# Kernel tuning notes

Hardware: AMD Instinct MI355X
Metric: run time of the kernel (lower is better)

## Reference

```python
import jax, jax.numpy as jnp
import numpy as np

NUM_HEADS = 12
EMB = 768
HEAD = 64
SEQ = 2048
BATCH = 2


def setup_inputs() -> dict:
    key = jax.random.key(0)
    ks = jax.random.split(key, 6)
    scale = 0.02
    x = jax.random.normal(ks[0], (BATCH, SEQ, EMB), dtype=jnp.float32)
    # per-head Q/K/V projections (bias-free, Karpathy-style HeadAttention), batched over heads
    Wq = jax.random.normal(ks[1], (NUM_HEADS, EMB, HEAD), dtype=jnp.float32) * scale
    Wk = jax.random.normal(ks[2], (NUM_HEADS, EMB, HEAD), dtype=jnp.float32) * scale
    Wv = jax.random.normal(ks[3], (NUM_HEADS, EMB, HEAD), dtype=jnp.float32) * scale
    # output projection: Linear(head_size*num_heads, emb_size)
    Wo = jax.random.normal(ks[4], (NUM_HEADS * HEAD, EMB), dtype=jnp.float32) * scale
    bo = jax.random.normal(ks[5], (EMB,), dtype=jnp.float32) * scale
    return {"x": x, "Wq": Wq, "Wk": Wk, "Wv": Wv, "Wo": Wo, "bo": bo}


def reference(x, Wq, Wk, Wv, Wo, bo):
    B, S, E = x.shape
    # batched per-head projections: [B,S,E] x [H,E,D] -> [B,H,S,D]
    q = jnp.einsum("bse,hed->bhsd", x, Wq)
    k = jnp.einsum("bse,hed->bhsd", x, Wk)
    v = jnp.einsum("bse,hed->bhsd", x, Wv)
    scale = 1.0 / jnp.sqrt(jnp.asarray(HEAD, dtype=x.dtype))
    scores = jnp.einsum("bhsd,bhtd->bhst", q, k) * scale  # [B,H,S,S]
    causal = jnp.tril(jnp.ones((S, S), dtype=bool))
    scores = jnp.where(causal, scores, jnp.asarray(-jnp.inf, dtype=scores.dtype))
    attn = jax.nn.softmax(scores, axis=-1)
    out = jnp.einsum("bhst,bhtd->bhsd", attn, v)  # [B,H,S,D]
    # concat heads along last dim: [B,S,H*D]
    out = out.transpose(0, 2, 1, 3).reshape(B, S, NUM_HEADS * HEAD)
    # output projection (dropout is identity in eval mode)
    return out @ Wo + bo
```

## Files before the change

### kernel.cpp

```cpp
#include <hip/hip_runtime.h>

#define NHEAD 12
#define EMB 768
#define HDD 64
#define SEQ 2048

typedef __attribute__((ext_vector_type(4))) float f32x4;
typedef __attribute__((ext_vector_type(8))) short short8;
typedef unsigned int u32;

#define GLL16(g, l)                                                            \
    __builtin_amdgcn_global_load_lds(                                          \
        (const __attribute__((address_space(1))) u32*)(g),                     \
        (__attribute__((address_space(3))) u32*)(l), 16, 0, 0)

static __device__ __forceinline__ short bf16s(float f) {
    unsigned u = __builtin_bit_cast(unsigned, f);
    u = (u + 0x7fffu + ((u >> 16) & 1u)) >> 16;
    return (short)u;
}

__global__ void k_cvt_x(const float* __restrict__ x, short* __restrict__ xb) {
    const int i = (blockIdx.x * 256 + threadIdx.x) * 8;
    const f32x4* s = (const f32x4*)(x + i);
    f32x4 a = s[0], b = s[1];
    short8 o;
    o[0] = bf16s(a[0]); o[1] = bf16s(a[1]); o[2] = bf16s(a[2]); o[3] = bf16s(a[3]);
    o[4] = bf16s(b[0]); o[5] = bf16s(b[1]); o[6] = bf16s(b[2]); o[7] = bf16s(b[3]);
    *(short8*)(xb + i) = o;
}

__global__ void k_cvt_whead(const float* __restrict__ Wq, const float* __restrict__ Wk,
                            const float* __restrict__ Wv, short* __restrict__ WqT,
                            short* __restrict__ WkT, short* __restrict__ WvT) {
    const float* W = blockIdx.z == 0 ? Wq : (blockIdx.z == 1 ? Wk : Wv);
    short* Wt = blockIdx.z == 0 ? WqT : (blockIdx.z == 1 ? WkT : WvT);
    __shared__ float tile[64][65];
    const int h = blockIdx.x, e0 = blockIdx.y * 64;
    const int t = threadIdx.x;
    const int r = t >> 2, c0 = (t & 3) * 16;
    const float* src = W + (h * EMB + e0 + r) * HDD + c0;
#pragma unroll
    for (int i = 0; i < 16; ++i) tile[r][c0 + i] = src[i];
    __syncthreads();
    short* dst = Wt + (h * HDD + r) * EMB + e0 + c0;
#pragma unroll
    for (int i = 0; i < 16; ++i) dst[i] = bf16s(tile[c0 + i][r]);
}

__global__ void k_cvt_wo(const float* __restrict__ W, short* __restrict__ Wt) {
    __shared__ float tile[64][65];
    const int k0 = blockIdx.x * 64, n0 = blockIdx.y * 64;
    const int t = threadIdx.x;
    const int r = t >> 2, c0 = (t & 3) * 16;
    const float* src = W + (k0 + r) * EMB + n0 + c0;
#pragma unroll
    for (int i = 0; i < 16; ++i) tile[r][c0 + i] = src[i];
    __syncthreads();
    short* dst = Wt + (n0 + r) * EMB + k0 + c0;
#pragma unroll
    for (int i = 0; i < 16; ++i) dst[i] = bf16s(tile[c0 + i][r]);
}

template <int MODE>
__global__ __launch_bounds__(256) void k_gemm(
        const short* __restrict__ xb, const short* __restrict__ Wt0,
        const short* __restrict__ Wt1, const short* __restrict__ Wt2,
        short* __restrict__ Qo, short* __restrict__ Ko, short* __restrict__ Vo,
        const float* __restrict__ bias, float* __restrict__ Fout) {
    __shared__ alignas(16) short As[128 * 32];
    __shared__ alignas(16) short Bs[128 * 32];
    const int t = threadIdx.x, lane = t & 63, wave = t >> 6;
    const int z = (MODE == 0) ? blockIdx.z : 0;
    const short* Ap;
    const short* Bp;
    int m0, n0;
    if (MODE == 1) {
        Ap = xb; Bp = Wt0; m0 = blockIdx.y * 128; n0 = blockIdx.x * 128;
    } else if (z == 0) {
        Ap = xb; Bp = Wt0; m0 = blockIdx.y * 128; n0 = blockIdx.x * 128;
    } else if (z == 1) {
        Ap = xb; Bp = Wt1; m0 = blockIdx.y * 128; n0 = blockIdx.x * 128;
    } else {
        Ap = Wt2; Bp = xb; m0 = blockIdx.x * 128; n0 = blockIdx.y * 128;
    }

    const short* gA = Ap + (long)(m0 + wave * 32 + (lane >> 2)) * EMB + (lane & 3) * 8;
    const short* gB = Bp + (long)(n0 + wave * 32 + (lane >> 2)) * EMB + (lane & 3) * 8;
    short* lA = As + (wave * 32) * 32;
    short* lB = Bs + (wave * 32) * 32;

    const int wm = (wave >> 1) * 64, wn = (wave & 1) * 64;
    const int fr = lane & 15, hi = lane >> 4, fk = hi * 8;

    f32x4 acc[4][4];
#pragma unroll
    for (int i = 0; i < 4; ++i)
#pragma unroll
        for (int j = 0; j < 4; ++j)
#pragma unroll
            for (int e = 0; e < 4; ++e) acc[i][j][e] = 0.f;

    for (int kk = 0; kk < EMB; kk += 32) {
        __syncthreads();
        GLL16(gA + kk, lA);
        GLL16(gA + kk + 16 * EMB, lA + 16 * 32);
        GLL16(gB + kk, lB);
        GLL16(gB + kk + 16 * EMB, lB + 16 * 32);
        __syncthreads();
        short8 af[4], bfq[4];
#pragma unroll
        for (int i = 0; i < 4; ++i)
            af[i] = *(const short8*)(As + (wm + i * 16 + fr) * 32 + fk);
#pragma unroll
        for (int j = 0; j < 4; ++j)
            bfq[j] = *(const short8*)(Bs + (wn + j * 16 + fr) * 32 + fk);
#pragma unroll
        for (int i = 0; i < 4; ++i)
#pragma unroll
            for (int j = 0; j < 4; ++j)
                acc[i][j] = __builtin_amdgcn_mfma_f32_16x16x32_bf16(af[i], bfq[j], acc[i][j], 0, 0, 0);
    }

    const int r0 = hi * 4;
#pragma unroll
    for (int i = 0; i < 4; ++i) {
#pragma unroll
        for (int j = 0; j < 4; ++j) {
            const int nbase = n0 + wn + j * 16 + fr;
            float bj = 0.f;
            if (MODE == 1) bj = bias[nbase];
#pragma unroll
            for (int r = 0; r < 4; ++r) {
                const int m = m0 + wm + i * 16 + r0 + r;
                float v = acc[i][j][r];
                if (MODE == 0) {
                    if (z == 2) {
                        const int hh = m >> 6, dd = m & 63;
                        const int bb = nbase >> 11, ss = nbase & 2047;
                        Vo[(long)((bb * NHEAD + hh) * HDD + dd) * SEQ + ss] = bf16s(v);
                    } else {
                        const int bb = m >> 11, ss = m & 2047;
                        const int hh = nbase >> 6, dd = nbase & 63;
                        short* Dst = (z == 0) ? Qo : Ko;
                        if (z == 0) v *= 0.125f;
                        Dst[(long)((bb * NHEAD + hh) * SEQ + ss) * HDD + dd] = bf16s(v);
                    }
                } else {
                    Fout[(long)m * EMB + nbase] = v + bj;
                }
            }
        }
    }
}

__global__ __launch_bounds__(512) void k_attn(
        const short* __restrict__ Q, const short* __restrict__ K,
        const short* __restrict__ VT, short* __restrict__ O) {
    __shared__ alignas(16) short Kbuf[2][64 * 72];
    __shared__ alignas(16) short Vbuf[2][64 * 72];
    __shared__ alignas(16) short Ps[8][16 * 72];
    const int bh = blockIdx.x;
    const int h = bh % NHEAD, b = bh / NHEAD;
    const int qs = (int)gridDim.y - 1 - (int)blockIdx.y;
    const int q0 = qs * 128;
    const int ntile = 2 * qs + 2;
    const int t = threadIdx.x, lane = t & 63, wave = t >> 6;
    const long base = (long)(b * NHEAD + h) * SEQ * HDD;
    const short* Qg = Q + base;
    const short* Kg = K + base;
    const short* Vg = VT + base;
    const int fr = lane & 15, hi = lane >> 4, fk = hi * 8, r0 = hi * 4;
    const int wq = q0 + wave * 16;

    short8 qf[2];
#pragma unroll
    for (int c = 0; c < 2; ++c)
        qf[c] = *(const short8*)(Qg + (long)(wq + fr) * HDD + c * 32 + fk);

    f32x4 oacc[4];
#pragma unroll
    for (int i = 0; i < 4; ++i)
#pragma unroll
        for (int e = 0; e < 4; ++e) oacc[i][e] = 0.f;
    float mrun = -3e38f, lrun = 0.f;

    const int srow = t >> 3, scol = (t & 7) * 8;
    const short* KgS = Kg + (long)srow * HDD + scol;
    const short* VgS = Vg + (long)srow * SEQ + scol;
    short* Pw = &Ps[wave][0];

    short8 kvR = *(const short8*)(KgS);
    short8 vvR = *(const short8*)(VgS);
    *(short8*)(&Kbuf[0][srow * 72 + scol]) = kvR;
    *(short8*)(&Vbuf[0][srow * 72 + scol]) = vvR;
    if (ntile > 1) {
        kvR = *(const short8*)(KgS + (long)64 * HDD);
        vvR = *(const short8*)(VgS + 64);
    }
    __syncthreads();

    for (int kt = 0; kt < ntile; ++kt) {
        const int k0 = kt * 64;
        const int cur = kt & 1;
        if (kt + 1 < ntile) {
            *(short8*)(&Kbuf[cur ^ 1][srow * 72 + scol]) = kvR;
            *(short8*)(&Vbuf[cur ^ 1][srow * 72 + scol]) = vvR;
            if (kt + 2 < ntile) {
                kvR = *(const short8*)(KgS + (long)(k0 + 128) * HDD);
                vvR = *(const short8*)(VgS + (k0 + 128));
            }
        }
        if (k0 <= wq + 15) {
            const short* Ks = &Kbuf[cur][0];
            const short* Vs = &Vbuf[cur][0];

            f32x4 st[4];
#pragma unroll
            for (int nt = 0; nt < 4; ++nt) {
                const short8 kf0 = *(const short8*)(Ks + (nt * 16 + fr) * 72 + fk);
                const short8 kf1 = *(const short8*)(Ks + (nt * 16 + fr) * 72 + 32 + fk);
#pragma unroll
                for (int e = 0; e < 4; ++e) st[nt][e] = 0.f;
                st[nt] = __builtin_amdgcn_mfma_f32_16x16x32_bf16(kf0, qf[0], st[nt], 0, 0, 0);
                st[nt] = __builtin_amdgcn_mfma_f32_16x16x32_bf16(kf1, qf[1], st[nt], 0, 0, 0);
            }

            float p[4][4];
            float pmax = -3e38f;
            if (k0 + 63 > wq) {
                const int myq = wq + fr;
#pragma unroll
                for (int nt = 0; nt < 4; ++nt)
#pragma unroll
                    for (int r = 0; r < 4; ++r) {
                        float s = st[nt][r];
                        if (k0 + nt * 16 + r0 + r > myq) s = -3e38f;
                        p[nt][r] = s;
                        pmax = fmaxf(pmax, s);
                    }
            } else {
#pragma unroll
                for (int nt = 0; nt < 4; ++nt)
#pragma unroll
                    for (int r = 0; r < 4; ++r) {
                        p[nt][r] = st[nt][r];
                        pmax = fmaxf(pmax, st[nt][r]);
                    }
            }
            pmax = fmaxf(pmax, __shfl_xor(pmax, 16, 64));
            pmax = fmaxf(pmax, __shfl_xor(pmax, 32, 64));
            const float mnew = fmaxf(mrun, pmax);
            const float corr = __expf(mrun - mnew);
            mrun = mnew;
            float rsum = 0.f;
#pragma unroll
            for (int nt = 0; nt < 4; ++nt)
#pragma unroll
                for (int r = 0; r < 4; ++r) {
                    const float e = __expf(p[nt][r] - mnew);
                    p[nt][r] = e;
                    rsum += e;
                }
            rsum += __shfl_xor(rsum, 16, 64);
            rsum += __shfl_xor(rsum, 32, 64);
            lrun = lrun * corr + rsum;
#pragma unroll
            for (int dt = 0; dt < 4; ++dt)
#pragma unroll
                for (int e = 0; e < 4; ++e) oacc[dt][e] *= corr;

#pragma unroll
            for (int nt = 0; nt < 4; ++nt)
#pragma unroll
                for (int r = 0; r < 4; ++r)
                    Pw[fr * 72 + nt * 16 + r0 + r] = bf16s(p[nt][r]);

#pragma unroll
            for (int kc = 0; kc < 2; ++kc) {
                const short8 pf = *(const short8*)(Pw + fr * 72 + kc * 32 + fk);
#pragma unroll
                for (int dt = 0; dt < 4; ++dt) {
                    const short8 vf = *(const short8*)(Vs + (dt * 16 + fr) * 72 + kc * 32 + fk);
                    oacc[dt] = __builtin_amdgcn_mfma_f32_16x16x32_bf16(vf, pf, oacc[dt], 0, 0, 0);
                }
            }
        }
        __syncthreads();
    }

    short* Os = &Ps[0][0];
    const float iv = 1.0f / lrun;
#pragma unroll
    for (int dt = 0; dt < 4; ++dt)
#pragma unroll
        for (int r = 0; r < 4; ++r)
            Os[(wave * 16 + fr) * 72 + dt * 16 + r0 + r] = bf16s(oacc[dt][r] * iv);
    __syncthreads();
    {
        const int row = t >> 2, c0 = (t & 3) * 16;
        const short8 o0 = *(const short8*)(Os + row * 72 + c0);
        const short8 o1 = *(const short8*)(Os + row * 72 + c0 + 8);
        short* Og = O + (long)(b * SEQ + q0 + row) * EMB + h * HDD + c0;
        *(short8*)Og = o0;
        *(short8*)(Og + 8) = o1;
    }
}

extern "C" void kernel_launch(void* const* d_in, const int* in_sizes, int n_in,
                              void* d_out, int out_size, void* d_ws, size_t ws_size,
                              hipStream_t stream) {
    const float* x  = (const float*)d_in[0];
    const float* Wq = (const float*)d_in[1];
    const float* Wk = (const float*)d_in[2];
    const float* Wv = (const float*)d_in[3];
    const float* Wo = (const float*)d_in[4];
    const float* bo = (const float*)d_in[5];
    float* out = (float*)d_out;

    char* ws = (char*)d_ws;
    short* xb  = (short*)(ws + 0);
    short* WqT = (short*)(ws + 6291456);
    short* WkT = (short*)(ws + 7471104);
    short* WvT = (short*)(ws + 8650752);
    short* WoT = (short*)(ws + 9830400);
    short* Qb  = (short*)(ws + 11010048);
    short* Kb  = (short*)(ws + 17301504);
    short* VTb = (short*)(ws + 23592960);
    short* Ob  = (short*)(ws + 29884416);

    k_cvt_x<<<dim3(1536), dim3(256), 0, stream>>>(x, xb);
    k_cvt_whead<<<dim3(12, 12, 3), dim3(256), 0, stream>>>(Wq, Wk, Wv, WqT, WkT, WvT);
    k_cvt_wo<<<dim3(12, 12), dim3(256), 0, stream>>>(Wo, WoT);
    k_gemm<0><<<dim3(6, 32, 3), dim3(256), 0, stream>>>(
        xb, WqT, WkT, WvT, Qb, Kb, VTb, (const float*)nullptr, (float*)nullptr);
    k_attn<<<dim3(24, 16), dim3(512), 0, stream>>>(Qb, Kb, VTb, Ob);
    k_gemm<1><<<dim3(6, 32, 1), dim3(256), 0, stream>>>(
        Ob, WoT, (const short*)nullptr, (const short*)nullptr,
        (short*)nullptr, (short*)nullptr, (short*)nullptr, bo, out);
}
```

Measured before the change: 106.8 us.

## Widen GEMM K-tile with XOR-swizzled LDS, pair causal query blocks in attention

```diff
diff --git a/kernel.cpp b/kernel.cpp
--- a/kernel.cpp
+++ b/kernel.cpp
@@ -7,6 +7,7 @@
 
 typedef __attribute__((ext_vector_type(4))) float f32x4;
 typedef __attribute__((ext_vector_type(8))) short short8;
+typedef __attribute__((ext_vector_type(4))) short short4v;
 typedef unsigned int u32;
 
 #define GLL16(g, l)                                                            \
@@ -62,14 +63,15 @@
     for (int i = 0; i < 16; ++i) dst[i] = bf16s(tile[c0 + i][r]);
 }
 
+#define GBK 64
 template <int MODE>
 __global__ __launch_bounds__(256) void k_gemm(
         const short* __restrict__ xb, const short* __restrict__ Wt0,
         const short* __restrict__ Wt1, const short* __restrict__ Wt2,
         short* __restrict__ Qo, short* __restrict__ Ko, short* __restrict__ Vo,
         const float* __restrict__ bias, float* __restrict__ Fout) {
-    __shared__ alignas(16) short As[128 * 32];
-    __shared__ alignas(16) short Bs[128 * 32];
+    __shared__ alignas(16) short As[128 * GBK];
+    __shared__ alignas(16) short Bs[128 * GBK];
     const int t = threadIdx.x, lane = t & 63, wave = t >> 6;
     const int z = (MODE == 0) ? blockIdx.z : 0;
     const short* Ap;
@@ -85,13 +87,14 @@
         Ap = Wt2; Bp = xb; m0 = blockIdx.x * 128; n0 = blockIdx.y * 128;
     }
 
-    const short* gA = Ap + (long)(m0 + wave * 32 + (lane >> 2)) * EMB + (lane & 3) * 8;
-    const short* gB = Bp + (long)(n0 + wave * 32 + (lane >> 2)) * EMB + (lane & 3) * 8;
-    short* lA = As + (wave * 32) * 32;
-    short* lB = Bs + (wave * 32) * 32;
+    const int srow = lane >> 3;
+    const int scolSw = ((lane & 7) ^ (lane >> 3)) * 8;
+    const short* gA = Ap + (long)(m0 + wave * 32 + srow) * EMB + scolSw;
+    const short* gB = Bp + (long)(n0 + wave * 32 + srow) * EMB + scolSw;
 
     const int wm = (wave >> 1) * 64, wn = (wave & 1) * 64;
     const int fr = lane & 15, hi = lane >> 4, fk = hi * 8;
+    const int sxa = (fr & 7) << 3;
 
     f32x4 acc[4][4];
 #pragma unroll
@@ -101,25 +104,29 @@
 #pragma unroll
             for (int e = 0; e < 4; ++e) acc[i][j][e] = 0.f;
 
-    for (int kk = 0; kk < EMB; kk += 32) {
-        __syncthreads();
-        GLL16(gA + kk, lA);
-        GLL16(gA + kk + 16 * EMB, lA + 16 * 32);
-        GLL16(gB + kk, lB);
-        GLL16(gB + kk + 16 * EMB, lB + 16 * 32);
-        __syncthreads();
-        short8 af[4], bfq[4];
-#pragma unroll
-        for (int i = 0; i < 4; ++i)
-            af[i] = *(const short8*)(As + (wm + i * 16 + fr) * 32 + fk);
-#pragma unroll
-        for (int j = 0; j < 4; ++j)
-            bfq[j] = *(const short8*)(Bs + (wn + j * 16 + fr) * 32 + fk);
-#pragma unroll
-        for (int i = 0; i < 4; ++i)
+    for (int kk = 0; kk < EMB; kk += GBK) {
+        __syncthreads();
+#pragma unroll
+        for (int i = 0; i < 4; ++i) {
+            GLL16(gA + kk + i * 8 * EMB, As + (wave * 32 + i * 8) * GBK);
+            GLL16(gB + kk + i * 8 * EMB, Bs + (wave * 32 + i * 8) * GBK);
+        }
+        __syncthreads();
+#pragma unroll
+        for (int kc = 0; kc < GBK; kc += 32) {
+            short8 af[4], bfq[4];
+#pragma unroll
+            for (int i = 0; i < 4; ++i)
+                af[i] = *(const short8*)(As + (wm + i * 16 + fr) * GBK + ((kc + fk) ^ sxa));
 #pragma unroll
             for (int j = 0; j < 4; ++j)
-                acc[i][j] = __builtin_amdgcn_mfma_f32_16x16x32_bf16(af[i], bfq[j], acc[i][j], 0, 0, 0);
+                bfq[j] = *(const short8*)(Bs + (wn + j * 16 + fr) * GBK + ((kc + fk) ^ sxa));
+#pragma unroll
+            for (int i = 0; i < 4; ++i)
+#pragma unroll
+                for (int j = 0; j < 4; ++j)
+                    acc[i][j] = __builtin_amdgcn_mfma_f32_16x16x32_bf16(af[i], bfq[j], acc[i][j], 0, 0, 0);
+        }
     }
 
     const int r0 = hi * 4;
@@ -162,148 +169,157 @@
     __shared__ alignas(16) short Ps[8][16 * 72];
     const int bh = blockIdx.x;
     const int h = bh % NHEAD, b = bh / NHEAD;
-    const int qs = (int)gridDim.y - 1 - (int)blockIdx.y;
-    const int q0 = qs * 128;
-    const int ntile = 2 * qs + 2;
+    const int pairp = blockIdx.y;
     const int t = threadIdx.x, lane = t & 63, wave = t >> 6;
     const long base = (long)(b * NHEAD + h) * SEQ * HDD;
     const short* Qg = Q + base;
     const short* Kg = K + base;
     const short* Vg = VT + base;
     const int fr = lane & 15, hi = lane >> 4, fk = hi * 8, r0 = hi * 4;
-    const int wq = q0 + wave * 16;
-
-    short8 qf[2];
-#pragma unroll
-    for (int c = 0; c < 2; ++c)
-        qf[c] = *(const short8*)(Qg + (long)(wq + fr) * HDD + c * 32 + fk);
-
-    f32x4 oacc[4];
-#pragma unroll
-    for (int i = 0; i < 4; ++i)
-#pragma unroll
-        for (int e = 0; e < 4; ++e) oacc[i][e] = 0.f;
-    float mrun = -3e38f, lrun = 0.f;
-
     const int srow = t >> 3, scol = (t & 7) * 8;
     const short* KgS = Kg + (long)srow * HDD + scol;
     const short* VgS = Vg + (long)srow * SEQ + scol;
     short* Pw = &Ps[wave][0];
-
-    short8 kvR = *(const short8*)(KgS);
-    short8 vvR = *(const short8*)(VgS);
-    *(short8*)(&Kbuf[0][srow * 72 + scol]) = kvR;
-    *(short8*)(&Vbuf[0][srow * 72 + scol]) = vvR;
-    if (ntile > 1) {
-        kvR = *(const short8*)(KgS + (long)64 * HDD);
-        vvR = *(const short8*)(VgS + 64);
-    }
-    __syncthreads();
-
-    for (int kt = 0; kt < ntile; ++kt) {
-        const int k0 = kt * 64;
-        const int cur = kt & 1;
-        if (kt + 1 < ntile) {
-            *(short8*)(&Kbuf[cur ^ 1][srow * 72 + scol]) = kvR;
-            *(short8*)(&Vbuf[cur ^ 1][srow * 72 + scol]) = vvR;
-            if (kt + 2 < ntile) {
-                kvR = *(const short8*)(KgS + (long)(k0 + 128) * HDD);
-                vvR = *(const short8*)(VgS + (k0 + 128));
+    short* Os = &Ps[0][0];
+
+#pragma unroll
+    for (int ph = 0; ph < 2; ++ph) {
+        const int qs = ph == 0 ? 15 - pairp : pairp;
+        const int q0 = qs * 128;
+        const int ntile = 2 * qs + 2;
+        const int wq = q0 + wave * 16;
+
+        short8 qf[2];
+#pragma unroll
+        for (int c = 0; c < 2; ++c)
+            qf[c] = *(const short8*)(Qg + (long)(wq + fr) * HDD + c * 32 + fk);
+
+        f32x4 oacc[4];
+#pragma unroll
+        for (int i = 0; i < 4; ++i)
+#pragma unroll
+            for (int e = 0; e < 4; ++e) oacc[i][e] = 0.f;
+        float mrun = -3e38f, lrun = 0.f;
+
+        short8 kvR = *(const short8*)(KgS);
+        short8 vvR = *(const short8*)(VgS);
+        *(short8*)(&Kbuf[0][srow * 72 + scol]) = kvR;
+        *(short8*)(&Vbuf[0][srow * 72 + scol]) = vvR;
+        if (ntile > 1) {
+            kvR = *(const short8*)(KgS + (long)64 * HDD);
+            vvR = *(const short8*)(VgS + 64);
+        }
+        __syncthreads();
+
+        for (int kt = 0; kt < ntile; ++kt) {
+            const int k0 = kt * 64;
+            const int cur = kt & 1;
+            if (kt + 1 < ntile) {
+                *(short8*)(&Kbuf[cur ^ 1][srow * 72 + scol]) = kvR;
+                *(short8*)(&Vbuf[cur ^ 1][srow * 72 + scol]) = vvR;
+                if (kt + 2 < ntile) {
+                    kvR = *(const short8*)(KgS + (long)(k0 + 128) * HDD);
+                    vvR = *(const short8*)(VgS + (k0 + 128));
+                }
             }
-        }
-        if (k0 <= wq + 15) {
-            const short* Ks = &Kbuf[cur][0];
-            const short* Vs = &Vbuf[cur][0];
-
-            f32x4 st[4];
-#pragma unroll
-            for (int nt = 0; nt < 4; ++nt) {
-                const short8 kf0 = *(const short8*)(Ks + (nt * 16 + fr) * 72 + fk);
-                const short8 kf1 = *(const short8*)(Ks + (nt * 16 + fr) * 72 + 32 + fk);
-#pragma unroll
-                for (int e = 0; e < 4; ++e) st[nt][e] = 0.f;
-                st[nt] = __builtin_amdgcn_mfma_f32_16x16x32_bf16(kf0, qf[0], st[nt], 0, 0, 0);
-                st[nt] = __builtin_amdgcn_mfma_f32_16x16x32_bf16(kf1, qf[1], st[nt], 0, 0, 0);
+            if (k0 <= wq + 15) {
+                const short* Ks = &Kbuf[cur][0];
+                const short* Vs = &Vbuf[cur][0];
+
+                f32x4 st[4];
+#pragma unroll
+                for (int nt = 0; nt < 4; ++nt) {
+                    const short8 kf0 = *(const short8*)(Ks + (nt * 16 + fr) * 72 + fk);
+                    const short8 kf1 = *(const short8*)(Ks + (nt * 16 + fr) * 72 + 32 + fk);
+#pragma unroll
+                    for (int e = 0; e < 4; ++e) st[nt][e] = 0.f;
+                    st[nt] = __builtin_amdgcn_mfma_f32_16x16x32_bf16(kf0, qf[0], st[nt], 0, 0, 0);
+                    st[nt] = __builtin_amdgcn_mfma_f32_16x16x32_bf16(kf1, qf[1], st[nt], 0, 0, 0);
+                }
+
+                float p[4][4];
+                float pmax = -3e38f;
+                if (k0 + 63 > wq) {
+                    const int myq = wq + fr;
+#pragma unroll
+                    for (int nt = 0; nt < 4; ++nt)
+#pragma unroll
+                        for (int r = 0; r < 4; ++r) {
+                            float s = st[nt][r];
+                            if (k0 + nt * 16 + r0 + r > myq) s = -3e38f;
+                            p[nt][r] = s;
+                            pmax = fmaxf(pmax, s);
+                        }
+                } else {
+#pragma unroll
+                    for (int nt = 0; nt < 4; ++nt)
+#pragma unroll
+                        for (int r = 0; r < 4; ++r) {
+                            p[nt][r] = st[nt][r];
+                            pmax = fmaxf(pmax, st[nt][r]);
+                        }
+                }
+                pmax = fmaxf(pmax, __shfl_xor(pmax, 16, 64));
+                pmax = fmaxf(pmax, __shfl_xor(pmax, 32, 64));
+                const float mnew = fmaxf(mrun, pmax);
+                const float corr = __expf(mrun - mnew);
+                mrun = mnew;
+                float rsum = 0.f;
+#pragma unroll
+                for (int nt = 0; nt < 4; ++nt)
+#pragma unroll
+                    for (int r = 0; r < 4; ++r) {
+                        const float e = __expf(p[nt][r] - mnew);
+                        p[nt][r] = e;
+                        rsum += e;
+                    }
+                rsum += __shfl_xor(rsum, 16, 64);
+                rsum += __shfl_xor(rsum, 32, 64);
+                lrun = lrun * corr + rsum;
+#pragma unroll
+                for (int dt = 0; dt < 4; ++dt)
+#pragma unroll
+                    for (int e = 0; e < 4; ++e) oacc[dt][e] *= corr;
+
+#pragma unroll
+                for (int nt = 0; nt < 4; ++nt) {
+                    short4v pk;
+                    pk[0] = bf16s(p[nt][0]);
+                    pk[1] = bf16s(p[nt][1]);
+                    pk[2] = bf16s(p[nt][2]);
+                    pk[3] = bf16s(p[nt][3]);
+                    *(short4v*)(Pw + fr * 72 + nt * 16 + r0) = pk;
+                }
+
+#pragma unroll
+                for (int kc = 0; kc < 2; ++kc) {
+                    const short8 pf = *(const short8*)(Pw + fr * 72 + kc * 32 + fk);
+#pragma unroll
+                    for (int dt = 0; dt < 4; ++dt) {
+                        const short8 vf = *(const short8*)(Vs + (dt * 16 + fr) * 72 + kc * 32 + fk);
+                        oacc[dt] = __builtin_amdgcn_mfma_f32_16x16x32_bf16(vf, pf, oacc[dt], 0, 0, 0);
+                    }
+                }
             }
-
-            float p[4][4];
-            float pmax = -3e38f;
-            if (k0 + 63 > wq) {
-                const int myq = wq + fr;
-#pragma unroll
-                for (int nt = 0; nt < 4; ++nt)
-#pragma unroll
-                    for (int r = 0; r < 4; ++r) {
-                        float s = st[nt][r];
-                        if (k0 + nt * 16 + r0 + r > myq) s = -3e38f;
-                        p[nt][r] = s;
-                        pmax = fmaxf(pmax, s);
-                    }
-            } else {
-#pragma unroll
-                for (int nt = 0; nt < 4; ++nt)
-#pragma unroll
-                    for (int r = 0; r < 4; ++r) {
-                        p[nt][r] = st[nt][r];
-                        pmax = fmaxf(pmax, st[nt][r]);
-                    }
-            }
-            pmax = fmaxf(pmax, __shfl_xor(pmax, 16, 64));
-            pmax = fmaxf(pmax, __shfl_xor(pmax, 32, 64));
-            const float mnew = fmaxf(mrun, pmax);
-            const float corr = __expf(mrun - mnew);
-            mrun = mnew;
-            float rsum = 0.f;
-#pragma unroll
-            for (int nt = 0; nt < 4; ++nt)
-#pragma unroll
-                for (int r = 0; r < 4; ++r) {
-                    const float e = __expf(p[nt][r] - mnew);
-                    p[nt][r] = e;
-                    rsum += e;
-                }
-            rsum += __shfl_xor(rsum, 16, 64);
-            rsum += __shfl_xor(rsum, 32, 64);
-            lrun = lrun * corr + rsum;
-#pragma unroll
-            for (int dt = 0; dt < 4; ++dt)
-#pragma unroll
-                for (int e = 0; e < 4; ++e) oacc[dt][e] *= corr;
-
-#pragma unroll
-            for (int nt = 0; nt < 4; ++nt)
-#pragma unroll
-                for (int r = 0; r < 4; ++r)
-                    Pw[fr * 72 + nt * 16 + r0 + r] = bf16s(p[nt][r]);
-
-#pragma unroll
-            for (int kc = 0; kc < 2; ++kc) {
-                const short8 pf = *(const short8*)(Pw + fr * 72 + kc * 32 + fk);
-#pragma unroll
-                for (int dt = 0; dt < 4; ++dt) {
-                    const short8 vf = *(const short8*)(Vs + (dt * 16 + fr) * 72 + kc * 32 + fk);
-                    oacc[dt] = __builtin_amdgcn_mfma_f32_16x16x32_bf16(vf, pf, oacc[dt], 0, 0, 0);
-                }
-            }
-        }
-        __syncthreads();
-    }
-
-    short* Os = &Ps[0][0];
-    const float iv = 1.0f / lrun;
-#pragma unroll
-    for (int dt = 0; dt < 4; ++dt)
-#pragma unroll
-        for (int r = 0; r < 4; ++r)
-            Os[(wave * 16 + fr) * 72 + dt * 16 + r0 + r] = bf16s(oacc[dt][r] * iv);
-    __syncthreads();
-    {
-        const int row = t >> 2, c0 = (t & 3) * 16;
-        const short8 o0 = *(const short8*)(Os + row * 72 + c0);
-        const short8 o1 = *(const short8*)(Os + row * 72 + c0 + 8);
-        short* Og = O + (long)(b * SEQ + q0 + row) * EMB + h * HDD + c0;
-        *(short8*)Og = o0;
-        *(short8*)(Og + 8) = o1;
+            __syncthreads();
+        }
+
+        const float iv = 1.0f / lrun;
+#pragma unroll
+        for (int dt = 0; dt < 4; ++dt)
+#pragma unroll
+            for (int r = 0; r < 4; ++r)
+                Os[(wave * 16 + fr) * 72 + dt * 16 + r0 + r] = bf16s(oacc[dt][r] * iv);
+        __syncthreads();
+        {
+            const int row = t >> 2, c0 = (t & 3) * 16;
+            const short8 o0 = *(const short8*)(Os + row * 72 + c0);
+            const short8 o1 = *(const short8*)(Os + row * 72 + c0 + 8);
+            short* Og = O + (long)(b * SEQ + q0 + row) * EMB + h * HDD + c0;
+            *(short8*)Og = o0;
+            *(short8*)(Og + 8) = o1;
+        }
+        __syncthreads();
     }
 }
 
@@ -334,7 +350,7 @@
     k_cvt_wo<<<dim3(12, 12), dim3(256), 0, stream>>>(Wo, WoT);
     k_gemm<0><<<dim3(6, 32, 3), dim3(256), 0, stream>>>(
         xb, WqT, WkT, WvT, Qb, Kb, VTb, (const float*)nullptr, (float*)nullptr);
-    k_attn<<<dim3(24, 16), dim3(512), 0, stream>>>(Qb, Kb, VTb, Ob);
+    k_attn<<<dim3(24, 8), dim3(512), 0, stream>>>(Qb, Kb, VTb, Ob);
     k_gemm<1><<<dim3(6, 32, 1), dim3(256), 0, stream>>>(
         Ob, WoT, (const short*)nullptr, (const short*)nullptr,
         (short*)nullptr, (short*)nullptr, (short*)nullptr, bo, out);
```

Measured after the change: 114.2 us. +6.9%, slower.

## Stream K/V tiles via global_load_lds with XOR-swizzled LDS layout

Applied to the files above, without the earlier changes.

```diff
diff --git a/kernel.cpp b/kernel.cpp
--- a/kernel.cpp
+++ b/kernel.cpp
@@ -7,6 +7,7 @@
 
 typedef __attribute__((ext_vector_type(4))) float f32x4;
 typedef __attribute__((ext_vector_type(8))) short short8;
+typedef __attribute__((ext_vector_type(4))) short short4v;
 typedef unsigned int u32;
 
 #define GLL16(g, l)                                                            \
@@ -157,8 +158,8 @@
 __global__ __launch_bounds__(512) void k_attn(
         const short* __restrict__ Q, const short* __restrict__ K,
         const short* __restrict__ VT, short* __restrict__ O) {
-    __shared__ alignas(16) short Kbuf[2][64 * 72];
-    __shared__ alignas(16) short Vbuf[2][64 * 72];
+    __shared__ alignas(16) short Kbuf[2][64 * 64];
+    __shared__ alignas(16) short Vbuf[2][64 * 64];
     __shared__ alignas(16) short Ps[8][16 * 72];
     const int bh = blockIdx.x;
     const int h = bh % NHEAD, b = bh / NHEAD;
@@ -185,31 +186,25 @@
         for (int e = 0; e < 4; ++e) oacc[i][e] = 0.f;
     float mrun = -3e38f, lrun = 0.f;
 
-    const int srow = t >> 3, scol = (t & 7) * 8;
-    const short* KgS = Kg + (long)srow * HDD + scol;
-    const short* VgS = Vg + (long)srow * SEQ + scol;
+    const int srow = t >> 3;
+    const int scolSw = ((t & 7) ^ (srow & 7)) * 8;
+    const short* KgS = Kg + (long)srow * HDD + scolSw;
+    const short* VgS = Vg + (long)srow * SEQ + scolSw;
+    const int ldst = wave * 512;
     short* Pw = &Ps[wave][0];
-
-    short8 kvR = *(const short8*)(KgS);
-    short8 vvR = *(const short8*)(VgS);
-    *(short8*)(&Kbuf[0][srow * 72 + scol]) = kvR;
-    *(short8*)(&Vbuf[0][srow * 72 + scol]) = vvR;
-    if (ntile > 1) {
-        kvR = *(const short8*)(KgS + (long)64 * HDD);
-        vvR = *(const short8*)(VgS + 64);
-    }
+    short* Os = &Ps[0][0];
+    const int rx = fr & 7;
+
+    GLL16(KgS, &Kbuf[0][ldst]);
+    GLL16(VgS, &Vbuf[0][ldst]);
     __syncthreads();
 
     for (int kt = 0; kt < ntile; ++kt) {
         const int k0 = kt * 64;
         const int cur = kt & 1;
         if (kt + 1 < ntile) {
-            *(short8*)(&Kbuf[cur ^ 1][srow * 72 + scol]) = kvR;
-            *(short8*)(&Vbuf[cur ^ 1][srow * 72 + scol]) = vvR;
-            if (kt + 2 < ntile) {
-                kvR = *(const short8*)(KgS + (long)(k0 + 128) * HDD);
-                vvR = *(const short8*)(VgS + (k0 + 128));
-            }
+            GLL16(KgS + (long)(k0 + 64) * HDD, &Kbuf[cur ^ 1][ldst]);
+            GLL16(VgS + (k0 + 64), &Vbuf[cur ^ 1][ldst]);
         }
         if (k0 <= wq + 15) {
             const short* Ks = &Kbuf[cur][0];
@@ -218,12 +213,14 @@
             f32x4 st[4];
 #pragma unroll
             for (int nt = 0; nt < 4; ++nt) {
-                const short8 kf0 = *(const short8*)(Ks + (nt * 16 + fr) * 72 + fk);
-                const short8 kf1 = *(const short8*)(Ks + (nt * 16 + fr) * 72 + 32 + fk);
+                const short8 kf0 = *(const short8*)(Ks + (nt * 16 + fr) * 64 + ((0 + hi) ^ rx) * 8);
+                const short8 kf1 = *(const short8*)(Ks + (nt * 16 + fr) * 64 + ((4 + hi) ^ rx) * 8);
 #pragma unroll
                 for (int e = 0; e < 4; ++e) st[nt][e] = 0.f;
+                __builtin_amdgcn_s_setprio(1);
                 st[nt] = __builtin_amdgcn_mfma_f32_16x16x32_bf16(kf0, qf[0], st[nt], 0, 0, 0);
                 st[nt] = __builtin_amdgcn_mfma_f32_16x16x32_bf16(kf1, qf[1], st[nt], 0, 0, 0);
+                __builtin_amdgcn_s_setprio(0);
             }
 
             float p[4][4];
@@ -271,25 +268,30 @@
                 for (int e = 0; e < 4; ++e) oacc[dt][e] *= corr;
 
 #pragma unroll
-            for (int nt = 0; nt < 4; ++nt)
-#pragma unroll
-                for (int r = 0; r < 4; ++r)
-                    Pw[fr * 72 + nt * 16 + r0 + r] = bf16s(p[nt][r]);
+            for (int nt = 0; nt < 4; ++nt) {
+                short4v pk;
+                pk[0] = bf16s(p[nt][0]);
+                pk[1] = bf16s(p[nt][1]);
+                pk[2] = bf16s(p[nt][2]);
+                pk[3] = bf16s(p[nt][3]);
+                *(short4v*)(Pw + fr * 72 + nt * 16 + r0) = pk;
+            }
 
 #pragma unroll
             for (int kc = 0; kc < 2; ++kc) {
                 const short8 pf = *(const short8*)(Pw + fr * 72 + kc * 32 + fk);
 #pragma unroll
                 for (int dt = 0; dt < 4; ++dt) {
-                    const short8 vf = *(const short8*)(Vs + (dt * 16 + fr) * 72 + kc * 32 + fk);
+                    const short8 vf = *(const short8*)(Vs + (dt * 16 + fr) * 64 + ((kc * 4 + hi) ^ rx) * 8);
+                    __builtin_amdgcn_s_setprio(1);
                     oacc[dt] = __builtin_amdgcn_mfma_f32_16x16x32_bf16(vf, pf, oacc[dt], 0, 0, 0);
+                    __builtin_amdgcn_s_setprio(0);
                 }
             }
         }
         __syncthreads();
     }
 
-    short* Os = &Ps[0][0];
     const float iv = 1.0f / lrun;
 #pragma unroll
     for (int dt = 0; dt < 4; ++dt)
```

Measured after the change: 112.9 us. 5.7% more time.
